# Performance work log

Hardware: AMD Instinct MI355X
Metric: run time of the kernel (lower is better)

Reference implementation:

```python
import jax, jax.numpy as jnp
import numpy as np

NSIDE = 64
NPIX = 12 * NSIDE * NSIDE  # hp.nside2npix(64) = 49152
B, C, N = 8, 16, 524288    # C = in_features - 2


def setup_inputs() -> dict:
    key = jax.random.key(0)
    k1, k2 = jax.random.split(key)
    vals = jax.random.normal(k1, (B, C, N), dtype=jnp.float32)
    pix = jax.random.randint(k2, (B, N), 0, NPIX, dtype=jnp.int32)
    return {"vals": vals, "pix": pix}


def reference(vals, pix):
    # Faithful to the torch loop: pooled[b, p, :] += vals[b, 0, i] (scalar from
    # channel 0 broadcast over all C output channels), counts[b, p] += 1,
    # counts clamped to >= 1, then mean.
    b_off = NPIX * jnp.arange(B, dtype=pix.dtype)[:, None]          # [B,1]
    flat_idx = (pix + b_off).reshape(-1)                            # [B*N]
    v0 = vals[:, 0, :].reshape(-1)                                  # [B*N]
    seg = jax.ops.segment_sum(v0, flat_idx, num_segments=B * NPIX)
    cnt = jax.ops.segment_sum(jnp.ones_like(v0), flat_idx, num_segments=B * NPIX)
    seg = seg.reshape(B, NPIX)
    cnt = jnp.maximum(cnt.reshape(B, NPIX), 1.0)
    pooled = jnp.broadcast_to((seg / cnt)[:, :, None], (B, NPIX, C))
    return pooled
```

## Files before the change

### kernel.cpp

```cpp
#include <hip/hip_runtime.h>

#define NSIDE 64
#define NPIX  (12 * NSIDE * NSIDE)
#define BATCH 8
#define CH    16
#define NPTS  524288

#define BIN_SHIFT 7
#define BPB   128
#define BINS  (NPIX / BPB)
#define NBINS (BATCH * BINS)
#define CAP   2048
#define CAP_SHIFT 11
#define WGS_PER_BATCH 64
#define SLICE (NPTS / WGS_PER_BATCH)
#define QSCALE 262144.0f
#define QMAX   ((1 << 24) - 1)

#define REC_OFFSET 16384

__global__ void hpx_init_cursors(unsigned int* __restrict__ cursor) {
    int i = blockIdx.x * blockDim.x + threadIdx.x;
    if (i < NBINS) cursor[i] = 0u;
}

__global__ __launch_bounds__(256) void hpx_partition(const float* __restrict__ vals,
                                                     const int* __restrict__ pix,
                                                     unsigned int* __restrict__ cursor,
                                                     unsigned int* __restrict__ rec) {
    __shared__ unsigned int hist[BINS];
    __shared__ unsigned int start[BINS];
    __shared__ unsigned int cur[BINS];
    __shared__ unsigned int gbase[BINS];
    __shared__ unsigned int gsum[24];
    __shared__ unsigned int srec[SLICE];

    const int wg  = blockIdx.x;
    const int b   = wg >> 6;
    const int s   = wg & (WGS_PER_BATCH - 1);
    const int tid = threadIdx.x;

    for (int i = tid; i < BINS; i += 256) { hist[i] = 0u; cur[i] = 0u; }
    __syncthreads();

    const int*   pixb = pix  + (size_t)b * NPTS + (size_t)s * SLICE;
    const float* valb = vals + (size_t)b * (CH * (size_t)NPTS) + (size_t)s * SLICE;

    int4 pr[8];
    #pragma unroll
    for (int it = 0; it < 8; ++it) {
        pr[it] = *(const int4*)(pixb + it * 1024 + tid * 4);
        atomicAdd(&hist[pr[it].x >> BIN_SHIFT], 1u);
        atomicAdd(&hist[pr[it].y >> BIN_SHIFT], 1u);
        atomicAdd(&hist[pr[it].z >> BIN_SHIFT], 1u);
        atomicAdd(&hist[pr[it].w >> BIN_SHIFT], 1u);
    }
    __syncthreads();

    if (tid < 24) {
        unsigned int acc = 0;
        #pragma unroll
        for (int k = 0; k < 16; ++k) {
            unsigned int h = hist[tid * 16 + k];
            start[tid * 16 + k] = acc;
            acc += h;
        }
        gsum[tid] = acc;
    }
    __syncthreads();
    if (tid == 0) {
        unsigned int a = 0;
        #pragma unroll
        for (int k = 0; k < 24; ++k) { unsigned int t = gsum[k]; gsum[k] = a; a += t; }
    }
    __syncthreads();
    for (int i = tid; i < BINS; i += 256) {
        start[i] += gsum[i >> 4];
        gbase[i] = atomicAdd(&cursor[b * BINS + i], hist[i]);
    }
    __syncthreads();

    #pragma unroll
    for (int it = 0; it < 8; ++it) {
        float4 v4 = *(const float4*)(valb + it * 1024 + tid * 4);
        int   p[4] = {pr[it].x, pr[it].y, pr[it].z, pr[it].w};
        float v[4] = {v4.x, v4.y, v4.z, v4.w};
        #pragma unroll
        for (int k = 0; k < 4; ++k) {
            int bin = p[k] >> BIN_SHIFT;
            unsigned int pos = start[bin] + atomicAdd(&cur[bin], 1u);
            int q = (int)lrintf(v[k] * QSCALE);
            q = q > QMAX ? QMAX : (q < -QMAX ? -QMAX : q);
            srec[pos] = ((unsigned int)(p[k] & (BPB - 1)) << 25) | ((unsigned int)q & 0x1FFFFFFu);
        }
    }
    __syncthreads();

    const int wave = tid >> 6, lane = tid & 63;
    for (int bin = wave; bin < BINS; bin += 4) {
        unsigned int n  = hist[bin];
        unsigned int s0 = start[bin];
        unsigned int g0 = gbase[bin];
        size_t rb = ((size_t)(b * BINS + bin)) << CAP_SHIFT;
        for (unsigned int j = lane; j < n; j += 64) {
            unsigned int gpos = g0 + j;
            if (gpos < CAP) rec[rb + gpos] = srec[s0 + j];
        }
    }
}

__global__ __launch_bounds__(256) void hpx_reduce(const unsigned int* __restrict__ rec,
                                                  const unsigned int* __restrict__ cursor,
                                                  float4* __restrict__ out) {
    __shared__ int          isum[BPB];
    __shared__ unsigned int icnt[BPB];
    __shared__ float        mean[BPB];

    const int wg  = blockIdx.x;
    const int b   = wg / BINS;
    const int bin = wg % BINS;
    const int tid = threadIdx.x;

    if (tid < BPB) { isum[tid] = 0; icnt[tid] = 0u; }
    __syncthreads();

    unsigned int n = cursor[wg];
    if (n > CAP) n = CAP;
    const unsigned int* r = rec + ((size_t)wg << CAP_SHIFT);

    unsigned int n4 = n & ~3u;
    for (unsigned int i = tid * 4; i < n4; i += 1024) {
        uint4 a = *(const uint4*)(r + i);
        unsigned int u[4] = {a.x, a.y, a.z, a.w};
        #pragma unroll
        for (int k = 0; k < 4; ++k) {
            unsigned int bkt = u[k] >> 25;
            int sv = ((int)(u[k] << 7)) >> 7;
            atomicAdd(&isum[bkt], sv);
            atomicAdd(&icnt[bkt], 1u);
        }
    }
    for (unsigned int i = n4 + tid; i < n; i += 256) {
        unsigned int u = r[i];
        unsigned int bkt = u >> 25;
        int sv = ((int)(u << 7)) >> 7;
        atomicAdd(&isum[bkt], sv);
        atomicAdd(&icnt[bkt], 1u);
    }
    __syncthreads();

    if (tid < BPB) {
        unsigned int c = icnt[tid];
        mean[tid] = (float)isum[tid] * (1.0f / QSCALE) / (float)(c ? c : 1u);
    }
    __syncthreads();

    size_t obase = ((size_t)b * NPIX + (size_t)bin * BPB) * 4;
    #pragma unroll
    for (int q = 0; q < 2; ++q) {
        int idx = q * 256 + tid;
        float m = mean[idx >> 2];
        out[obase + idx] = make_float4(m, m, m, m);
    }
}

#define SUM_SCALE 16777216.0f
#define CNT_SHIFT 44

__global__ void hpx_zero_ws(unsigned long long* __restrict__ acc, int n) {
    int i = blockIdx.x * blockDim.x + threadIdx.x;
    if (i < n) acc[i] = 0ULL;
}

__global__ void hpx_scatter(const float* __restrict__ vals,
                            const int* __restrict__ pix,
                            unsigned long long* __restrict__ acc) {
    int t = blockIdx.x * blockDim.x + threadIdx.x;
    int e0 = t * 4;
    if (e0 >= BATCH * NPTS) return;
    int b = e0 >> 19;
    int j = e0 & (NPTS - 1);
    int4   p4 = *(const int4*)(pix + e0);
    float4 v4 = *(const float4*)(vals + (size_t)b * (CH * (size_t)NPTS) + j);
    const unsigned long long one = 1ULL << CNT_SHIFT;
    int base = b * NPIX;
    long long s0 = (long long)llrintf(v4.x * SUM_SCALE);
    long long s1 = (long long)llrintf(v4.y * SUM_SCALE);
    long long s2 = (long long)llrintf(v4.z * SUM_SCALE);
    long long s3 = (long long)llrintf(v4.w * SUM_SCALE);
    atomicAdd(&acc[base + p4.x], one + (unsigned long long)s0);
    atomicAdd(&acc[base + p4.y], one + (unsigned long long)s1);
    atomicAdd(&acc[base + p4.z], one + (unsigned long long)s2);
    atomicAdd(&acc[base + p4.w], one + (unsigned long long)s3);
}

__global__ void hpx_finalize(const unsigned long long* __restrict__ acc,
                             float4* __restrict__ out) {
    int t = blockIdx.x * blockDim.x + threadIdx.x;
    if (t >= BATCH * NPIX * 4) return;
    int bp = t >> 2;
    unsigned long long a = acc[bp];
    long long s = ((long long)(a << (64 - CNT_SHIFT))) >> (64 - CNT_SHIFT);
    unsigned int c = (unsigned int)((a - (unsigned long long)s) >> CNT_SHIFT);
    float denom = (float)(c > 0u ? c : 1u);
    float m = (float)((double)s * (1.0 / (double)SUM_SCALE)) / denom;
    out[t] = make_float4(m, m, m, m);
}

extern "C" void kernel_launch(void* const* d_in, const int* in_sizes, int n_in,
                              void* d_out, int out_size, void* d_ws, size_t ws_size,
                              hipStream_t stream) {
    const float* vals = (const float*)d_in[0];
    const int*   pix  = (const int*)d_in[1];
    float*       out  = (float*)d_out;

    const size_t need = (size_t)REC_OFFSET + (size_t)NBINS * CAP * sizeof(unsigned int);

    if (ws_size >= need) {
        unsigned int* cursor = (unsigned int*)d_ws;
        unsigned int* rec    = (unsigned int*)((char*)d_ws + REC_OFFSET);

        hpx_init_cursors<<<(NBINS + 255) / 256, 256, 0, stream>>>(cursor);
        hpx_partition<<<BATCH * WGS_PER_BATCH, 256, 0, stream>>>(vals, pix, cursor, rec);
        hpx_reduce<<<NBINS, 256, 0, stream>>>(rec, cursor, (float4*)out);
    } else {
        const int nbuckets = BATCH * NPIX;
        unsigned long long* acc = (unsigned long long*)d_ws;
        hpx_zero_ws<<<(nbuckets + 255) / 256, 256, 0, stream>>>(acc, nbuckets);
        int total_threads = (BATCH * NPTS) / 4;
        hpx_scatter<<<total_threads / 256, 256, 0, stream>>>(vals, pix, acc);
        int total = BATCH * NPIX * 4;
        hpx_finalize<<<(total + 255) / 256, 256, 0, stream>>>(acc, (float4*)out);
    }
}
```

Measured before the change: 343.6 us.

## Write per-workgroup sorted slices with offset table instead of global bin cursors

The partition kernel now writes each workgroup's locally bin-sorted records contiguously, coalesced with uint4 stores, and emits a per-workgroup bin offset table. This removes the global cursor atomics, the cursor-init kernel and the capped per-bin global buckets. Per-element ranks come from the histogram atomics, so the second shared-memory atomic pass is gone. The reduce kernel now gathers its bin's segment from 64 source slices with a single 64-bit packed count+sum shared atomic, which adds 64 small scattered reads per bin in exchange.

```diff
diff --git a/kernel.cpp b/kernel.cpp
--- a/kernel.cpp
+++ b/kernel.cpp
@@ -10,28 +10,21 @@
 #define BPB   128
 #define BINS  (NPIX / BPB)
 #define NBINS (BATCH * BINS)
-#define CAP   2048
-#define CAP_SHIFT 11
 #define WGS_PER_BATCH 64
+#define NWG   (BATCH * WGS_PER_BATCH)
 #define SLICE (NPTS / WGS_PER_BATCH)
 #define QSCALE 262144.0f
 #define QMAX   ((1 << 24) - 1)
 
-#define REC_OFFSET 16384
-
-__global__ void hpx_init_cursors(unsigned int* __restrict__ cursor) {
-    int i = blockIdx.x * blockDim.x + threadIdx.x;
-    if (i < NBINS) cursor[i] = 0u;
-}
+#define TBL_STRIDE 512
+#define REC_OFFSET (1u << 20)
 
 __global__ __launch_bounds__(256) void hpx_partition(const float* __restrict__ vals,
                                                      const int* __restrict__ pix,
-                                                     unsigned int* __restrict__ cursor,
+                                                     unsigned int* __restrict__ table,
                                                      unsigned int* __restrict__ rec) {
     __shared__ unsigned int hist[BINS];
     __shared__ unsigned int start[BINS];
-    __shared__ unsigned int cur[BINS];
-    __shared__ unsigned int gbase[BINS];
     __shared__ unsigned int gsum[24];
     __shared__ unsigned int srec[SLICE];
 
@@ -40,20 +33,21 @@
     const int s   = wg & (WGS_PER_BATCH - 1);
     const int tid = threadIdx.x;
 
-    for (int i = tid; i < BINS; i += 256) { hist[i] = 0u; cur[i] = 0u; }
+    for (int i = tid; i < BINS; i += 256) hist[i] = 0u;
     __syncthreads();
 
     const int*   pixb = pix  + (size_t)b * NPTS + (size_t)s * SLICE;
     const float* valb = vals + (size_t)b * (CH * (size_t)NPTS) + (size_t)s * SLICE;
 
     int4 pr[8];
+    unsigned short rank[32];
     #pragma unroll
     for (int it = 0; it < 8; ++it) {
         pr[it] = *(const int4*)(pixb + it * 1024 + tid * 4);
-        atomicAdd(&hist[pr[it].x >> BIN_SHIFT], 1u);
-        atomicAdd(&hist[pr[it].y >> BIN_SHIFT], 1u);
-        atomicAdd(&hist[pr[it].z >> BIN_SHIFT], 1u);
-        atomicAdd(&hist[pr[it].w >> BIN_SHIFT], 1u);
+        rank[it * 4 + 0] = (unsigned short)atomicAdd(&hist[pr[it].x >> BIN_SHIFT], 1u);
+        rank[it * 4 + 1] = (unsigned short)atomicAdd(&hist[pr[it].y >> BIN_SHIFT], 1u);
+        rank[it * 4 + 2] = (unsigned short)atomicAdd(&hist[pr[it].z >> BIN_SHIFT], 1u);
+        rank[it * 4 + 3] = (unsigned short)atomicAdd(&hist[pr[it].w >> BIN_SHIFT], 1u);
     }
     __syncthreads();
 
@@ -74,10 +68,7 @@
         for (int k = 0; k < 24; ++k) { unsigned int t = gsum[k]; gsum[k] = a; a += t; }
     }
     __syncthreads();
-    for (int i = tid; i < BINS; i += 256) {
-        start[i] += gsum[i >> 4];
-        gbase[i] = atomicAdd(&cursor[b * BINS + i], hist[i]);
-    }
+    for (int i = tid; i < BINS; i += 256) start[i] += gsum[i >> 4];
     __syncthreads();
 
     #pragma unroll
@@ -88,7 +79,7 @@
         #pragma unroll
         for (int k = 0; k < 4; ++k) {
             int bin = p[k] >> BIN_SHIFT;
-            unsigned int pos = start[bin] + atomicAdd(&cur[bin], 1u);
+            unsigned int pos = start[bin] + (unsigned int)rank[it * 4 + k];
             int q = (int)lrintf(v[k] * QSCALE);
             q = q > QMAX ? QMAX : (q < -QMAX ? -QMAX : q);
             srec[pos] = ((unsigned int)(p[k] & (BPB - 1)) << 25) | ((unsigned int)q & 0x1FFFFFFu);
@@ -96,62 +87,51 @@
     }
     __syncthreads();
 
-    const int wave = tid >> 6, lane = tid & 63;
-    for (int bin = wave; bin < BINS; bin += 4) {
-        unsigned int n  = hist[bin];
-        unsigned int s0 = start[bin];
-        unsigned int g0 = gbase[bin];
-        size_t rb = ((size_t)(b * BINS + bin)) << CAP_SHIFT;
-        for (unsigned int j = lane; j < n; j += 64) {
-            unsigned int gpos = g0 + j;
-            if (gpos < CAP) rec[rb + gpos] = srec[s0 + j];
-        }
+    {
+        const uint4* s4 = (const uint4*)srec;
+        uint4* r4 = (uint4*)(rec + (size_t)wg * SLICE);
+        #pragma unroll
+        for (int it = 0; it < (SLICE / 4) / 256; ++it)
+            r4[it * 256 + tid] = s4[it * 256 + tid];
+        for (int i = tid; i < BINS + 1; i += 256)
+            table[(size_t)wg * TBL_STRIDE + i] = (i < BINS) ? start[i] : (unsigned int)SLICE;
     }
 }
 
 __global__ __launch_bounds__(256) void hpx_reduce(const unsigned int* __restrict__ rec,
-                                                  const unsigned int* __restrict__ cursor,
+                                                  const unsigned int* __restrict__ table,
                                                   float4* __restrict__ out) {
-    __shared__ int          isum[BPB];
-    __shared__ unsigned int icnt[BPB];
-    __shared__ float        mean[BPB];
+    __shared__ unsigned long long acc[BPB];
+    __shared__ float mean[BPB];
 
     const int wg  = blockIdx.x;
     const int b   = wg / BINS;
     const int bin = wg % BINS;
     const int tid = threadIdx.x;
 
-    if (tid < BPB) { isum[tid] = 0; icnt[tid] = 0u; }
-    __syncthreads();
-
-    unsigned int n = cursor[wg];
-    if (n > CAP) n = CAP;
-    const unsigned int* r = rec + ((size_t)wg << CAP_SHIFT);
-
-    unsigned int n4 = n & ~3u;
-    for (unsigned int i = tid * 4; i < n4; i += 1024) {
-        uint4 a = *(const uint4*)(r + i);
-        unsigned int u[4] = {a.x, a.y, a.z, a.w};
-        #pragma unroll
-        for (int k = 0; k < 4; ++k) {
-            unsigned int bkt = u[k] >> 25;
-            int sv = ((int)(u[k] << 7)) >> 7;
-            atomicAdd(&isum[bkt], sv);
-            atomicAdd(&icnt[bkt], 1u);
+    if (tid < BPB) acc[tid] = 0ULL;
+    __syncthreads();
+
+    const int wave = tid >> 6, lane = tid & 63;
+    for (int s = wave; s < WGS_PER_BATCH; s += 4) {
+        int srcwg = b * WGS_PER_BATCH + s;
+        unsigned int off = table[(size_t)srcwg * TBL_STRIDE + bin];
+        unsigned int end = table[(size_t)srcwg * TBL_STRIDE + bin + 1];
+        const unsigned int* r = rec + (size_t)srcwg * SLICE;
+        for (unsigned int j = off + lane; j < end; j += 64) {
+            unsigned int u = r[j];
+            unsigned int bkt = u >> 25;
+            long long sv = ((int)(u << 7)) >> 7;
+            atomicAdd(&acc[bkt], (1ULL << 44) + (unsigned long long)sv);
         }
     }
-    for (unsigned int i = n4 + tid; i < n; i += 256) {
-        unsigned int u = r[i];
-        unsigned int bkt = u >> 25;
-        int sv = ((int)(u << 7)) >> 7;
-        atomicAdd(&isum[bkt], sv);
-        atomicAdd(&icnt[bkt], 1u);
-    }
     __syncthreads();
 
     if (tid < BPB) {
-        unsigned int c = icnt[tid];
-        mean[tid] = (float)isum[tid] * (1.0f / QSCALE) / (float)(c ? c : 1u);
+        unsigned long long a = acc[tid];
+        long long sv = ((long long)(a << 20)) >> 20;
+        unsigned int c = (unsigned int)((a - (unsigned long long)sv) >> 44);
+        mean[tid] = (float)sv * (1.0f / QSCALE) / (float)(c ? c : 1u);
     }
     __syncthreads();
 
@@ -167,14 +147,14 @@
 #define SUM_SCALE 16777216.0f
 #define CNT_SHIFT 44
 
-__global__ void hpx_zero_ws(unsigned long long* __restrict__ acc, int n) {
+__global__ void hpx_zero_ws(unsigned long long* __restrict__ accg, int n) {
     int i = blockIdx.x * blockDim.x + threadIdx.x;
-    if (i < n) acc[i] = 0ULL;
+    if (i < n) accg[i] = 0ULL;
 }
 
 __global__ void hpx_scatter(const float* __restrict__ vals,
                             const int* __restrict__ pix,
-                            unsigned long long* __restrict__ acc) {
+                            unsigned long long* __restrict__ accg) {
     int t = blockIdx.x * blockDim.x + threadIdx.x;
     int e0 = t * 4;
     if (e0 >= BATCH * NPTS) return;
@@ -188,18 +168,18 @@
     long long s1 = (long long)llrintf(v4.y * SUM_SCALE);
     long long s2 = (long long)llrintf(v4.z * SUM_SCALE);
     long long s3 = (long long)llrintf(v4.w * SUM_SCALE);
-    atomicAdd(&acc[base + p4.x], one + (unsigned long long)s0);
-    atomicAdd(&acc[base + p4.y], one + (unsigned long long)s1);
-    atomicAdd(&acc[base + p4.z], one + (unsigned long long)s2);
-    atomicAdd(&acc[base + p4.w], one + (unsigned long long)s3);
-}
-
-__global__ void hpx_finalize(const unsigned long long* __restrict__ acc,
+    atomicAdd(&accg[base + p4.x], one + (unsigned long long)s0);
+    atomicAdd(&accg[base + p4.y], one + (unsigned long long)s1);
+    atomicAdd(&accg[base + p4.z], one + (unsigned long long)s2);
+    atomicAdd(&accg[base + p4.w], one + (unsigned long long)s3);
+}
+
+__global__ void hpx_finalize(const unsigned long long* __restrict__ accg,
                              float4* __restrict__ out) {
     int t = blockIdx.x * blockDim.x + threadIdx.x;
     if (t >= BATCH * NPIX * 4) return;
     int bp = t >> 2;
-    unsigned long long a = acc[bp];
+    unsigned long long a = accg[bp];
     long long s = ((long long)(a << (64 - CNT_SHIFT))) >> (64 - CNT_SHIFT);
     unsigned int c = (unsigned int)((a - (unsigned long long)s) >> CNT_SHIFT);
     float denom = (float)(c > 0u ? c : 1u);
@@ -214,22 +194,21 @@
     const int*   pix  = (const int*)d_in[1];
     float*       out  = (float*)d_out;
 
-    const size_t need = (size_t)REC_OFFSET + (size_t)NBINS * CAP * sizeof(unsigned int);
+    const size_t need = (size_t)REC_OFFSET + (size_t)NWG * SLICE * sizeof(unsigned int);
 
     if (ws_size >= need) {
-        unsigned int* cursor = (unsigned int*)d_ws;
-        unsigned int* rec    = (unsigned int*)((char*)d_ws + REC_OFFSET);
-
-        hpx_init_cursors<<<(NBINS + 255) / 256, 256, 0, stream>>>(cursor);
-        hpx_partition<<<BATCH * WGS_PER_BATCH, 256, 0, stream>>>(vals, pix, cursor, rec);
-        hpx_reduce<<<NBINS, 256, 0, stream>>>(rec, cursor, (float4*)out);
+        unsigned int* table = (unsigned int*)d_ws;
+        unsigned int* rec   = (unsigned int*)((char*)d_ws + REC_OFFSET);
+
+        hpx_partition<<<NWG, 256, 0, stream>>>(vals, pix, table, rec);
+        hpx_reduce<<<NBINS, 256, 0, stream>>>(rec, table, (float4*)out);
     } else {
         const int nbuckets = BATCH * NPIX;
-        unsigned long long* acc = (unsigned long long*)d_ws;
-        hpx_zero_ws<<<(nbuckets + 255) / 256, 256, 0, stream>>>(acc, nbuckets);
+        unsigned long long* accg = (unsigned long long*)d_ws;
+        hpx_zero_ws<<<(nbuckets + 255) / 256, 256, 0, stream>>>(accg, nbuckets);
         int total_threads = (BATCH * NPTS) / 4;
-        hpx_scatter<<<total_threads / 256, 256, 0, stream>>>(vals, pix, acc);
+        hpx_scatter<<<total_threads / 256, 256, 0, stream>>>(vals, pix, accg);
         int total = BATCH * NPIX * 4;
-        hpx_finalize<<<(total + 255) / 256, 256, 0, stream>>>(acc, (float4*)out);
-    }
-}
+        hpx_finalize<<<(total + 255) / 256, 256, 0, stream>>>(accg, (float4*)out);
+    }
+}
```

Result: no change. 339.2 us (-1.3%).
